# Kernel optimization log

Hardware: AMD Instinct MI355X
Metric: run time of the kernel (lower is better)

Reference implementation:

```python
import jax, jax.numpy as jnp
import numpy as np

CUR, FULL, BS, D = 1024, 2048, 4, 1024
HN, HD = 16, 64
PREV = FULL - CUR
SCALE = 1.0 / HD ** 0.5


def rel_shift(x):
    # x: (bs, hn, cur, full) -> TXL relative shift over last two dims
    b, h, q, k = x.shape
    x = jnp.pad(x, ((0, 0), (0, 0), (0, 0), (1, 0)))  # (b,h,q,k+1)
    x = x.reshape(b, h, k + 1, q)[:, :, 1:, :]
    return x.reshape(b, h, q, k)


def setup_inputs() -> dict:
    key = jax.random.key(0)
    ks = jax.random.split(key, 16)
    s = 0.02
    inputs = jax.random.normal(ks[0], (CUR, BS, D), jnp.float32)
    pos_embedding = jax.random.normal(ks[1], (FULL, 1, D), jnp.float32)
    full_input = jax.random.normal(ks[2], (FULL, BS, D), jnp.float32)
    # causal mask: query i (absolute pos i+PREV) cannot attend to key j > i+PREV
    i = jnp.arange(CUR)[:, None]
    j = jnp.arange(FULL)[None, :]
    mask = (j > i + PREV)[:, :, None]  # (cur, full, 1) bool
    W_kv = jax.random.normal(ks[3], (D, 2 * HN * HD), jnp.float32) * s
    b_kv = jnp.zeros((2 * HN * HD,), jnp.float32)
    W_q = jax.random.normal(ks[4], (D, HN * HD), jnp.float32) * s
    b_q = jnp.zeros((HN * HD,), jnp.float32)
    W_pos = jax.random.normal(ks[5], (D, HN * HD), jnp.float32) * s
    b_pos = jnp.zeros((HN * HD,), jnp.float32)
    W_proj = jax.random.normal(ks[6], (HN * HD, D), jnp.float32) * s
    b_proj = jnp.zeros((D,), jnp.float32)
    u = jax.random.normal(ks[7], (HN, HD), jnp.float32) * s
    v = jax.random.normal(ks[8], (HN, HD), jnp.float32) * s
    return dict(inputs=inputs, pos_embedding=pos_embedding, full_input=full_input,
                u=u, v=v, mask=mask, W_kv=W_kv, b_kv=b_kv, W_q=W_q, b_q=b_q,
                W_pos=W_pos, b_pos=b_pos, W_proj=W_proj, b_proj=b_proj)


def reference(inputs, pos_embedding, full_input, u, v, mask,
              W_kv, b_kv, W_q, b_q, W_pos, b_pos, W_proj, b_proj):
    cur, bs, _ = inputs.shape
    full = full_input.shape[0]
    kv = full_input @ W_kv + b_kv                      # (full, bs, 2*hn*hd)
    k, val = jnp.split(kv, 2, axis=-1)
    k = k.reshape(full, bs, HN, HD)
    val = val.reshape(full, bs, HN, HD)
    q = (inputs @ W_q + b_q).reshape(cur, bs, HN, HD)
    r = (pos_embedding @ W_pos + b_pos).reshape(full, HN, HD)
    content = jnp.einsum('ibhd,jbhd->bhij', q + u, k)   # (bs,hn,cur,full)
    position = jnp.einsum('ibhd,jhd->bhij', q + v, r)
    position = rel_shift(position)
    attn = (content + position) * SCALE
    attn = jnp.where(mask[None, :, :, 0][:, None, :, :], -jnp.inf, attn)
    attn = jax.nn.softmax(attn, axis=-1)
    out = jnp.einsum('bhij,jbhd->ibhd', attn, val).reshape(cur, bs, HN * HD)
    return out @ W_proj + b_proj
```

## Files before the change

kernel.cpp:

```cpp
#include <hip/hip_runtime.h>


typedef _Float16 half8 __attribute__((ext_vector_type(8)));
typedef _Float16 half4v __attribute__((ext_vector_type(4)));
typedef float f32x4 __attribute__((ext_vector_type(4)));

typedef const __attribute__((address_space(1))) void* gas_ptr;
typedef __attribute__((address_space(3))) void* las_ptr;

__device__ __forceinline__ void load_lds16(const void* g, void* l) {
  __builtin_amdgcn_global_load_lds((gas_ptr)g, (las_ptr)l, 16, 0, 0);
}

__global__ __launch_bounds__(256) void prep(
    const float* __restrict__ inputs, const float* __restrict__ full_inp,
    const float* __restrict__ pos_emb, const float* __restrict__ Wq,
    const float* __restrict__ Wkv, const float* __restrict__ Wpos,
    const float* __restrict__ Wproj, _Float16* __restrict__ o_in,
    _Float16* __restrict__ o_full, _Float16* __restrict__ o_pos,
    _Float16* __restrict__ owq, _Float16* __restrict__ owkv,
    _Float16* __restrict__ owpos, _Float16* __restrict__ owproj) {
  __shared__ _Float16 tile[64][65];
  const int bx = blockIdx.x;
  const int t = threadIdx.x;
  if (bx < 14336) {
    size_t g = (size_t)bx * 256 + t;
    const float* src;
    _Float16* dst;
    size_t sg;
    if (g < (1u << 20)) {
      const int rd = (int)(g >> 8), b = rd >> 10, i = rd & 1023;
      src = inputs; dst = o_in;
      sg = ((size_t)(i * 4 + b) << 8) + (g & 255);
    } else if (g < (3u << 20)) {
      const size_t gd = g - (1u << 20);
      const int rd = (int)(gd >> 8), b = rd >> 11, j = rd & 2047;
      src = full_inp; dst = o_full;
      sg = ((size_t)(j * 4 + b) << 8) + (gd & 255);
      float4 vv = *(const float4*)(src + sg * 4);
      half4v hh;
      hh[0] = (_Float16)vv.x; hh[1] = (_Float16)vv.y;
      hh[2] = (_Float16)vv.z; hh[3] = (_Float16)vv.w;
      *(half4v*)(dst + gd * 4) = hh;
      return;
    } else {
      const size_t gd = g - (3u << 20);
      float4 vv = *(const float4*)(pos_emb + gd * 4);
      half4v hh;
      hh[0] = (_Float16)vv.x; hh[1] = (_Float16)vv.y;
      hh[2] = (_Float16)vv.z; hh[3] = (_Float16)vv.w;
      *(half4v*)(o_pos + gd * 4) = hh;
      return;
    }
    float4 vv = *(const float4*)(src + sg * 4);
    half4v hh;
    hh[0] = (_Float16)vv.x; hh[1] = (_Float16)vv.y;
    hh[2] = (_Float16)vv.z; hh[3] = (_Float16)vv.w;
    *(half4v*)(dst + (g & ((1u << 20) - 1)) * 4) = hh;
    return;
  }
  const int wb = bx - 14336;
  const float* W;
  _Float16* Wt;
  int N, tidx;
  if (wb < 256) { W = Wq; Wt = owq; N = 1024; tidx = wb; }
  else if (wb < 768) { W = Wkv; Wt = owkv; N = 2048; tidx = wb - 256; }
  else if (wb < 1024) { W = Wpos; Wt = owpos; N = 1024; tidx = wb - 768; }
  else { W = Wproj; Wt = owproj; N = 1024; tidx = wb - 1024; }
  const int K = 1024;
  const int n0 = (tidx % (N >> 6)) * 64, k0 = (tidx / (N >> 6)) * 64;
  const int rr = t >> 2, cc = (t & 3) * 16;
#pragma unroll
  for (int i = 0; i < 4; ++i) {
    float4 v = *(const float4*)&W[(size_t)(k0 + rr) * N + n0 + cc + i * 4];
    tile[rr][cc + i * 4 + 0] = (_Float16)v.x;
    tile[rr][cc + i * 4 + 1] = (_Float16)v.y;
    tile[rr][cc + i * 4 + 2] = (_Float16)v.z;
    tile[rr][cc + i * 4 + 3] = (_Float16)v.w;
  }
  __syncthreads();
  const int n = t >> 2, kc = (t & 3) * 16;
#pragma unroll
  for (int i = 0; i < 4; ++i) {
    half4v h;
    h[0] = tile[kc + i * 4 + 0][n];
    h[1] = tile[kc + i * 4 + 1][n];
    h[2] = tile[kc + i * 4 + 2][n];
    h[3] = tile[kc + i * 4 + 3][n];
    *(half4v*)&Wt[(size_t)(n0 + n) * K + k0 + kc + i * 4] = h;
  }
}

__global__ __launch_bounds__(256, 2) void gemm3(
    const _Float16* __restrict__ Aq, const _Float16* __restrict__ Akv,
    const _Float16* __restrict__ Ar, const _Float16* __restrict__ Btq,
    const _Float16* __restrict__ Btkv, const _Float16* __restrict__ Btr,
    const float* __restrict__ bq, const float* __restrict__ bkv,
    const float* __restrict__ br, const float* __restrict__ uu,
    _Float16* __restrict__ qfu, _Float16* __restrict__ kf,
    _Float16* __restrict__ vfT, _Float16* __restrict__ rf) {
  __shared__ _Float16 smem[128 * 66];
  _Float16* As = smem;
  _Float16* Bs = smem + 4096;
  const int gb = blockIdx.x;
  const _Float16* A;
  const _Float16* Bt;
  const float* bias;
  int mode, bm, bn;
  if (gb < 256) {
    mode = 1; A = Aq; Bt = Btq; bias = bq;
    bn = (gb & 7) * 128; bm = (gb >> 3) * 128;
  } else if (gb < 1280) {
    mode = 2; A = Akv; Bt = Btkv; bias = bkv;
    const int j = gb - 256;
    bn = (j & 15) * 128; bm = (j >> 4) * 128;
  } else {
    mode = 3; A = Ar; Bt = Btr; bias = br;
    const int j = gb - 1280;
    bn = (j & 7) * 128; bm = (j >> 3) * 128;
  }
  const int K = 1024;
  const int t = threadIdx.x, w = t >> 6, l = t & 63;
  const int l15 = l & 15, l4 = l >> 4;
  const int wm = (w >> 1) * 64, wn = (w & 1) * 64;

  f32x4 acc[4][4];
  const f32x4 z4 = {0.f, 0.f, 0.f, 0.f};
#pragma unroll
  for (int i = 0; i < 4; ++i)
#pragma unroll
    for (int j = 0; j < 4; ++j) acc[i][j] = z4;

  const char* Abase = (const char*)A + (size_t)bm * K * 2;
  const char* Bbase = (const char*)Bt + (size_t)bn * K * 2;

  for (int k0 = 0; k0 < K; k0 += 32) {
    __syncthreads();
#pragma unroll
    for (int iss = 0; iss < 2; ++iss) {
      const int off = w * 1024 + iss * 4096 + l * 16;
      const int row = off >> 6, kb = off & 63;
      load_lds16(Abase + (size_t)row * (K * 2) + k0 * 2 + kb,
                 (char*)As + off);
      load_lds16(Bbase + (size_t)row * (K * 2) + k0 * 2 + kb,
                 (char*)Bs + off);
    }
    __syncthreads();
    half8 af[4], bf[4];
#pragma unroll
    for (int mt = 0; mt < 4; ++mt)
      af[mt] = *(const half8*)&As[(wm + mt * 16 + l15) * 32 + l4 * 8];
#pragma unroll
    for (int nt = 0; nt < 4; ++nt)
      bf[nt] = *(const half8*)&Bs[(wn + nt * 16 + l15) * 32 + l4 * 8];
#pragma unroll
    for (int mt = 0; mt < 4; ++mt)
#pragma unroll
      for (int nt = 0; nt < 4; ++nt)
        acc[mt][nt] = __builtin_amdgcn_mfma_f32_16x16x32_f16(
            af[mt], bf[nt], acc[mt][nt], 0, 0, 0);
  }

  if (mode == 2 && bn >= 1024) {
    const int b = bm >> 11, j0m = bm & 2047;
    const int hbase = (bn - 1024) >> 6;
#pragma unroll
    for (int ch = 0; ch < 2; ++ch) {
      __syncthreads();
      if (((wn >> 6) & 1) == ch) {
#pragma unroll
        for (int mt = 0; mt < 4; ++mt)
#pragma unroll
          for (int r = 0; r < 4; ++r) {
            const int rowl = wm + mt * 16 + l4 * 4 + r;
#pragma unroll
            for (int nt = 0; nt < 4; ++nt) {
              const int coll = nt * 16 + l15;
              smem[rowl * 66 + coll] =
                  (_Float16)(acc[mt][nt][r] + bias[bn + wn + coll]);
            }
          }
      }
      __syncthreads();
#pragma unroll
      for (int it = 0; it < 4; ++it) {
        const int c = t + 256 * it;
        const int d = c >> 4, ck = c & 15;
        half8 v8;
#pragma unroll
        for (int z = 0; z < 8; ++z) v8[z] = smem[(ck * 8 + z) * 66 + d];
        *(half8*)&vfT[(((size_t)(b * 16 + hbase + ch) * 64 + d) << 11) + j0m +
                      ck * 8] = v8;
      }
    }
    return;
  }

#pragma unroll
  for (int mt = 0; mt < 4; ++mt)
#pragma unroll
    for (int r = 0; r < 4; ++r) {
      const int rowl = wm + mt * 16 + l4 * 4 + r;
#pragma unroll
      for (int nt = 0; nt < 4; ++nt) {
        const int col = bn + wn + nt * 16 + l15;
        const float val = acc[mt][nt][r] + bias[col];
        if (mode == 1) {
          const int b = bm >> 10, i0m = bm & 1023;
          const int h = col >> 6, d = col & 63;
          qfu[(((size_t)(b * 16 + h) * 1024 + i0m + rowl) << 6) + d] =
              (_Float16)((val + uu[col]) * 0.125f);
        } else if (mode == 2) {
          const int b = bm >> 11, j0m = bm & 2047;
          const int h = col >> 6, d = col & 63;
          kf[(((size_t)(b * 16 + h) * 2048 + j0m + rowl) << 6) + d] =
              (_Float16)val;
        } else {
          const int h = col >> 6, d = col & 63;
          rf[(((size_t)h * 2048 + bm + rowl) << 6) + d] = (_Float16)val;
        }
      }
    }
}

__global__ __launch_bounds__(256, 2) void gemm_proj(
    const _Float16* __restrict__ A, const _Float16* __restrict__ Bt,
    const float* __restrict__ bias, float* __restrict__ out0, int M, int N,
    int K) {
  __shared__ _Float16 As[128 * 32];
  __shared__ _Float16 Bs[128 * 32];
  const int t = threadIdx.x, w = t >> 6, l = t & 63;
  const int l15 = l & 15, l4 = l >> 4;
  const int bm = blockIdx.y * 128, bn = blockIdx.x * 128;
  const int wm = (w >> 1) * 64, wn = (w & 1) * 64;

  f32x4 acc[4][4];
  const f32x4 z4 = {0.f, 0.f, 0.f, 0.f};
#pragma unroll
  for (int i = 0; i < 4; ++i)
#pragma unroll
    for (int j = 0; j < 4; ++j) acc[i][j] = z4;

  const char* Abase = (const char*)A + (size_t)bm * K * 2;
  const char* Bbase = (const char*)Bt + (size_t)bn * K * 2;

  for (int k0 = 0; k0 < K; k0 += 32) {
    __syncthreads();
#pragma unroll
    for (int iss = 0; iss < 2; ++iss) {
      const int off = w * 1024 + iss * 4096 + l * 16;
      const int row = off >> 6, kb = off & 63;
      load_lds16(Abase + (size_t)row * (K * 2) + k0 * 2 + kb,
                 (char*)As + off);
      load_lds16(Bbase + (size_t)row * (K * 2) + k0 * 2 + kb,
                 (char*)Bs + off);
    }
    __syncthreads();
    half8 af[4], bf[4];
#pragma unroll
    for (int mt = 0; mt < 4; ++mt)
      af[mt] = *(const half8*)&As[(wm + mt * 16 + l15) * 32 + l4 * 8];
#pragma unroll
    for (int nt = 0; nt < 4; ++nt)
      bf[nt] = *(const half8*)&Bs[(wn + nt * 16 + l15) * 32 + l4 * 8];
#pragma unroll
    for (int mt = 0; mt < 4; ++mt)
#pragma unroll
      for (int nt = 0; nt < 4; ++nt)
        acc[mt][nt] = __builtin_amdgcn_mfma_f32_16x16x32_f16(
            af[mt], bf[nt], acc[mt][nt], 0, 0, 0);
  }

#pragma unroll
  for (int mt = 0; mt < 4; ++mt)
#pragma unroll
    for (int r = 0; r < 4; ++r) {
      const int row = bm + wm + mt * 16 + l4 * 4 + r;
#pragma unroll
      for (int nt = 0; nt < 4; ++nt) {
        const int col = bn + wn + nt * 16 + l15;
        out0[(size_t)row * N + col] = acc[mt][nt][r] + bias[col];
      }
    }
}

__global__ __launch_bounds__(256, 2) void attn_mfma(
    const _Float16* __restrict__ qfu,
    const _Float16* __restrict__ kf,
    const _Float16* __restrict__ vfT,
    const _Float16* __restrict__ rf,
    const float* __restrict__ u,
    const float* __restrict__ v,
    _Float16* __restrict__ attn_out)
{
  __shared__ _Float16 ks[64 * 64];
  __shared__ _Float16 vts[64 * 64];
  __shared__ _Float16 rs[256 * 64];
  __shared__ _Float16 pA[2][4][16 * 64];

  const int t = threadIdx.x, w = t >> 6, l = t & 63;
  const int l15 = l & 15, l4 = l >> 4;
  const int id = blockIdx.x;
  const int bh = ((id >> 3) & 7) * 8 + (id & 7);
  const int qt = id >> 6;
  const int bx = (qt < 4) ? (7 - qt) : (qt - 4);
  const int i0 = bx * 128;
  const int h = bh & 15, b = bh >> 4;

  const char* kfb = (const char*)(kf + (((size_t)bh * 2048) << 6));
  const char* vg = (const char*)(vfT + (((size_t)bh) << 17));
  const char* rg = (const char*)(rf + (((size_t)h) << 17));

  half8 qa0[2], qa1[2], qv0[2], qv1[2];
  {
    half8 dl0, dl1;
#pragma unroll
    for (int z = 0; z < 8; ++z) {
      const int di = l4 * 8 + z;
      dl0[z] = (_Float16)(0.125f * (v[h * 64 + di] - u[h * 64 + di]));
      dl1[z] = (_Float16)(0.125f * (v[h * 64 + 32 + di] - u[h * 64 + 32 + di]));
    }
#pragma unroll
    for (int g = 0; g < 2; ++g) {
      const size_t qo =
          (((size_t)bh * 1024 + i0 + 64 * g + w * 16 + l15) << 6) + l4 * 8;
      qa0[g] = *(const half8*)(qfu + qo);
      qa1[g] = *(const half8*)(qfu + qo + 32);
      qv0[g] = qa0[g] + dl0;
      qv1[g] = qa1[g] + dl1;
    }
  }
  const f32x4 z4 = {0.f, 0.f, 0.f, 0.f};
  f32x4 o[2][4];
  float lsum[2][4];
#pragma unroll
  for (int g = 0; g < 2; ++g)
#pragma unroll
    for (int nt = 0; nt < 4; ++nt) { o[g][nt] = z4; lsum[g][nt] = 0.f; }

  const int mb0 = 960 - i0;
  const int njt = 2 * bx + 18;

#pragma unroll
  for (int iss = 0; iss < 6; ++iss) {
    const int off = w * 1024 + iss * 4096 + l * 16;
    const int q = off >> 7;
    const int cph = (off >> 4) & 7;
    const int slot = (mb0 - 64 + q) & 255;
    int m = mb0 - 64 + q;
    m = m < 2047 ? m : 2047;
    load_lds16(rg + (size_t)m * 128 + ((cph ^ (slot & 7)) << 4),
               (char*)rs + slot * 128 + cph * 16);
  }

  for (int jt = 0; jt < njt; ++jt) {
    const int j0 = jt * 64;
    const int m_base = j0 - i0 + 960;
    __syncthreads();
    {
      const char* kg = kfb + (size_t)j0 * 128;
#pragma unroll
      for (int iss = 0; iss < 2; ++iss) {
        const int off = w * 1024 + iss * 4096 + l * 16;
        const int row = off >> 7;
        const int cph = (off >> 4) & 7;
        const int sw = ((cph ^ (row & 7)) << 4);
        load_lds16(kg + (size_t)row * 128 + sw, (char*)ks + off);
        load_lds16(vg + (size_t)row * 4096 + (size_t)j0 * 2 + sw,
                   (char*)vts + off);
      }
    }
    if (jt > 0) {
      const int m0 = m_base + 64;
#pragma unroll
      for (int iss = 0; iss < 2; ++iss) {
        const int off = w * 1024 + iss * 4096 + l * 16;
        const int q = off >> 7;
        const int cph = (off >> 4) & 7;
        const int slot = (m0 + q) & 255;
        int m = m0 + q;
        m = m < 2047 ? m : 2047;
        load_lds16(rg + (size_t)m * 128 + ((cph ^ (slot & 7)) << 4),
                   (char*)rs + slot * 128 + cph * 16);
      }
    }
    __syncthreads();

    f32x4 sc[2][4];
#pragma unroll
    for (int nt = 0; nt < 4; ++nt) {
      const int row = nt * 16 + l15;
      const int rsw = row & 7;
      const half8 b0 = *(const half8*)&ks[row * 64 + ((l4 ^ rsw) * 8)];
      const half8 b1 = *(const half8*)&ks[row * 64 + (((4 + l4) ^ rsw) * 8)];
#pragma unroll
      for (int g = 0; g < 2; ++g) {
        f32x4 cc = z4;
        cc = __builtin_amdgcn_mfma_f32_16x16x32_f16(qa0[g], b0, cc, 0, 0, 0);
        cc = __builtin_amdgcn_mfma_f32_16x16x32_f16(qa1[g], b1, cc, 0, 0, 0);
        sc[g][nt] = cc;
      }
    }

#pragma unroll
    for (int g = 0; g < 2; ++g) {
      const int cw = i0 + 64 * g - j0 + 1024 + 16 * w;
      if (g == 0 && cw < -15) continue;
      const int mbg = m_base - 64 * g;
      f32x4 accP[5];
#pragma unroll
      for (int p = 0; p < 5; ++p) {
        const int m = mbg + (3 - w + p) * 16 + l15;
        const int slot = m & 255;
        const int ssw = slot & 7;
        const half8 b0 = *(const half8*)&rs[slot * 64 + ((l4 ^ ssw) * 8)];
        const half8 b1 = *(const half8*)&rs[slot * 64 + (((4 + l4) ^ ssw) * 8)];
        f32x4 cc = z4;
        cc = __builtin_amdgcn_mfma_f32_16x16x32_f16(qv0[g], b0, cc, 0, 0, 0);
        cc = __builtin_amdgcn_mfma_f32_16x16x32_f16(qv1[g], b1, cc, 0, 0, 0);
        accP[p] = cc;
      }
      if (cw >= 63) {
#pragma unroll
        for (int r = 0; r < 4; ++r) {
          const int thr = 4 * l4 + r;
          const int srcl = (l4 << 4) | ((15 + l15 - thr) & 15);
          float rot[5];
#pragma unroll
          for (int p = 0; p < 5; ++p) rot[p] = __shfl(accP[p][r], srcl, 64);
          float esum = 0.f;
          const int sw2 = (thr & 7) * 8;
#pragma unroll
          for (int nt = 0; nt < 4; ++nt) {
            const float pv = (l15 <= thr) ? rot[nt] : rot[nt + 1];
            const float e = __expf(sc[g][nt][r] + pv);
            esum += e;
            pA[g][w][thr * 64 + ((16 * nt + l15) ^ sw2)] = (_Float16)e;
          }
          lsum[g][r] += esum;
        }
      } else {
#pragma unroll
        for (int r = 0; r < 4; ++r) {
          const int thr = 4 * l4 + r;
          const int srcl = (l4 << 4) | ((15 + l15 - thr) & 15);
          float rot[5];
#pragma unroll
          for (int p = 0; p < 5; ++p) rot[p] = __shfl(accP[p][r], srcl, 64);
          float esum = 0.f;
          const int sw2 = (thr & 7) * 8;
#pragma unroll
          for (int nt = 0; nt < 4; ++nt) {
            const float pv = (l15 <= thr) ? rot[nt] : rot[nt + 1];
            const bool masked = (16 * nt + l15) > (cw + thr);
            const float e = masked ? 0.f : __expf(sc[g][nt][r] + pv);
            esum += e;
            pA[g][w][thr * 64 + ((16 * nt + l15) ^ sw2)] = (_Float16)e;
          }
          lsum[g][r] += esum;
        }
      }
    }

    const bool act0 = (i0 - j0 + 1024 + 16 * w) >= -15;
#pragma unroll
    for (int kk = 0; kk < 2; ++kk) {
      const int aoff = l15 * 64 + ((kk * 32 + l4 * 8) ^ ((l15 & 7) * 8));
      half8 a81 = *(const half8*)&pA[1][w][aoff];
      half8 a80;
      if (act0) a80 = *(const half8*)&pA[0][w][aoff];
#pragma unroll
      for (int nt = 0; nt < 4; ++nt) {
        const int row = nt * 16 + l15;
        const half8 b8 =
            *(const half8*)&vts[row * 64 + ((((kk << 2) + l4) ^ (row & 7)) * 8)];
        if (act0)
          o[0][nt] =
              __builtin_amdgcn_mfma_f32_16x16x32_f16(a80, b8, o[0][nt], 0, 0, 0);
        o[1][nt] =
            __builtin_amdgcn_mfma_f32_16x16x32_f16(a81, b8, o[1][nt], 0, 0, 0);
      }
    }
  }

#pragma unroll
  for (int g = 0; g < 2; ++g)
#pragma unroll
    for (int r = 0; r < 4; ++r) {
      float s = lsum[g][r];
      s += __shfl_xor(s, 1, 64);
      s += __shfl_xor(s, 2, 64);
      s += __shfl_xor(s, 4, 64);
      s += __shfl_xor(s, 8, 64);
      const float inv = 1.0f / s;
      const int i = i0 + 64 * g + w * 16 + l4 * 4 + r;
      const size_t base = ((size_t)i * 4 + b) * 1024 + h * 64;
#pragma unroll
      for (int nt = 0; nt < 4; ++nt)
        attn_out[base + nt * 16 + l15] = (_Float16)(o[g][nt][r] * inv);
    }
}

extern "C" void kernel_launch(void* const* d_in, const int* in_sizes, int n_in,
                              void* d_out, int out_size, void* d_ws,
                              size_t ws_size, hipStream_t stream) {
  const float* inputs   = (const float*)d_in[0];
  const float* pos_emb  = (const float*)d_in[1];
  const float* full_inp = (const float*)d_in[2];
  const float* u        = (const float*)d_in[3];
  const float* v        = (const float*)d_in[4];
  const float* W_kv   = (const float*)d_in[6];
  const float* b_kv   = (const float*)d_in[7];
  const float* W_q    = (const float*)d_in[8];
  const float* b_q    = (const float*)d_in[9];
  const float* W_pos  = (const float*)d_in[10];
  const float* b_pos  = (const float*)d_in[11];
  const float* W_proj = (const float*)d_in[12];
  const float* b_proj = (const float*)d_in[13];
  float* out = (float*)d_out;

  char* ws = (char*)d_ws;
  const size_t MB = 1024 * 1024;
  _Float16* in_q_h    = (_Float16*)(ws);
  _Float16* in_full_h = (_Float16*)(ws + 8 * MB);
  _Float16* in_pos_h  = (_Float16*)(ws + 24 * MB);
  _Float16* attn_h    = (_Float16*)(ws + 28 * MB);
  _Float16* wq_t      = (_Float16*)(ws + 36 * MB);
  _Float16* wkv_t     = (_Float16*)(ws + 38 * MB);
  _Float16* wpos_t    = (_Float16*)(ws + 42 * MB);
  _Float16* wproj_t   = (_Float16*)(ws + 44 * MB);
  _Float16* qfu       = (_Float16*)(ws + 46 * MB);
  _Float16* kf        = (_Float16*)(ws + 54 * MB);
  _Float16* vfT       = (_Float16*)(ws + 70 * MB);
  _Float16* rf        = (_Float16*)(ws + 86 * MB);

  const dim3 blk(256);
  prep<<<dim3(15616), blk, 0, stream>>>(inputs, full_inp, pos_emb, W_q, W_kv,
                                        W_pos, W_proj, in_q_h, in_full_h,
                                        in_pos_h, wq_t, wkv_t, wpos_t, wproj_t);
  gemm3<<<dim3(1408), blk, 0, stream>>>(in_q_h, in_full_h, in_pos_h, wq_t,
                                        wkv_t, wpos_t, b_q, b_kv, b_pos, u,
                                        qfu, kf, vfT, rf);
  attn_mfma<<<dim3(512), blk, 0, stream>>>(qfu, kf, vfT, rf, u, v, attn_h);
  gemm_proj<<<dim3(8, 32), blk, 0, stream>>>(attn_h, wproj_t, b_proj, out,
                                             4096, 1024, 1024);
}
```

Before: 333.1 us.

## Double GEMM K-tile to 64 with XOR-swizzled LDS and batch prep conversion

The two MFMA GEMM kernels now stage a 64-wide K slice per iteration instead of 32. This halves the number of barrier-synchronised load rounds. An XOR swizzle on 16-byte chunks in the global-to-LDS copy and the fragment reads is meant to avoid LDS bank conflicts with the wider rows. The prep kernel's elementwise fp32-to-fp16 conversion is also restructured so each of 2048 blocks handles 7 chunks in an unrolled loop, which cuts the block count. In exchange, LDS use per block doubles, which could limit occupancy.

```diff
diff --git a/kernel.cpp b/kernel.cpp
--- a/kernel.cpp
+++ b/kernel.cpp
@@ -23,43 +23,36 @@
   __shared__ _Float16 tile[64][65];
   const int bx = blockIdx.x;
   const int t = threadIdx.x;
-  if (bx < 14336) {
-    size_t g = (size_t)bx * 256 + t;
-    const float* src;
-    _Float16* dst;
-    size_t sg;
-    if (g < (1u << 20)) {
-      const int rd = (int)(g >> 8), b = rd >> 10, i = rd & 1023;
-      src = inputs; dst = o_in;
-      sg = ((size_t)(i * 4 + b) << 8) + (g & 255);
-    } else if (g < (3u << 20)) {
-      const size_t gd = g - (1u << 20);
-      const int rd = (int)(gd >> 8), b = rd >> 11, j = rd & 2047;
-      src = full_inp; dst = o_full;
-      sg = ((size_t)(j * 4 + b) << 8) + (gd & 255);
-      float4 vv = *(const float4*)(src + sg * 4);
+  if (bx < 2048) {
+#pragma unroll
+    for (int it = 0; it < 7; ++it) {
+      const size_t g = (size_t)bx * 256 + t + (size_t)it * (2048 * 256);
+      float4 vv;
+      _Float16* dptr;
+      if (g < (1u << 20)) {
+        const int rd = (int)(g >> 8), b = rd >> 10, i = rd & 1023;
+        const size_t sg = ((size_t)(i * 4 + b) << 8) + (g & 255);
+        vv = *(const float4*)(inputs + sg * 4);
+        dptr = o_in + g * 4;
+      } else if (g < (3u << 20)) {
+        const size_t gd = g - (1u << 20);
+        const int rd = (int)(gd >> 8), b = rd >> 11, j = rd & 2047;
+        const size_t sg = ((size_t)(j * 4 + b) << 8) + (gd & 255);
+        vv = *(const float4*)(full_inp + sg * 4);
+        dptr = o_full + gd * 4;
+      } else {
+        const size_t gd = g - (3u << 20);
+        vv = *(const float4*)(pos_emb + gd * 4);
+        dptr = o_pos + gd * 4;
+      }
       half4v hh;
       hh[0] = (_Float16)vv.x; hh[1] = (_Float16)vv.y;
       hh[2] = (_Float16)vv.z; hh[3] = (_Float16)vv.w;
-      *(half4v*)(dst + gd * 4) = hh;
-      return;
-    } else {
-      const size_t gd = g - (3u << 20);
-      float4 vv = *(const float4*)(pos_emb + gd * 4);
-      half4v hh;
-      hh[0] = (_Float16)vv.x; hh[1] = (_Float16)vv.y;
-      hh[2] = (_Float16)vv.z; hh[3] = (_Float16)vv.w;
-      *(half4v*)(o_pos + gd * 4) = hh;
-      return;
-    }
-    float4 vv = *(const float4*)(src + sg * 4);
-    half4v hh;
-    hh[0] = (_Float16)vv.x; hh[1] = (_Float16)vv.y;
-    hh[2] = (_Float16)vv.z; hh[3] = (_Float16)vv.w;
-    *(half4v*)(dst + (g & ((1u << 20) - 1)) * 4) = hh;
+      *(half4v*)dptr = hh;
+    }
     return;
   }
-  const int wb = bx - 14336;
+  const int wb = bx - 2048;
   const float* W;
   _Float16* Wt;
   int N, tidx;
@@ -99,9 +92,9 @@
     const float* __restrict__ br, const float* __restrict__ uu,
     _Float16* __restrict__ qfu, _Float16* __restrict__ kf,
     _Float16* __restrict__ vfT, _Float16* __restrict__ rf) {
-  __shared__ _Float16 smem[128 * 66];
+  __shared__ _Float16 smem[128 * 128];
   _Float16* As = smem;
-  _Float16* Bs = smem + 4096;
+  _Float16* Bs = smem + 8192;
   const int gb = blockIdx.x;
   const _Float16* A;
   const _Float16* Bt;
@@ -134,31 +127,34 @@
   const char* Abase = (const char*)A + (size_t)bm * K * 2;
   const char* Bbase = (const char*)Bt + (size_t)bn * K * 2;
 
-  for (int k0 = 0; k0 < K; k0 += 32) {
+  for (int k0 = 0; k0 < K; k0 += 64) {
     __syncthreads();
 #pragma unroll
-    for (int iss = 0; iss < 2; ++iss) {
-      const int off = w * 1024 + iss * 4096 + l * 16;
-      const int row = off >> 6, kb = off & 63;
-      load_lds16(Abase + (size_t)row * (K * 2) + k0 * 2 + kb,
-                 (char*)As + off);
-      load_lds16(Bbase + (size_t)row * (K * 2) + k0 * 2 + kb,
-                 (char*)Bs + off);
+    for (int iss = 0; iss < 4; ++iss) {
+      const int off = w * 4096 + iss * 1024 + l * 16;
+      const int row = off >> 7;
+      const int sw = ((((off >> 4) & 7) ^ (row & 7)) << 4);
+      load_lds16(Abase + (size_t)row * (K * 2) + k0 * 2 + sw, (char*)As + off);
+      load_lds16(Bbase + (size_t)row * (K * 2) + k0 * 2 + sw, (char*)Bs + off);
     }
     __syncthreads();
-    half8 af[4], bf[4];
-#pragma unroll
-    for (int mt = 0; mt < 4; ++mt)
-      af[mt] = *(const half8*)&As[(wm + mt * 16 + l15) * 32 + l4 * 8];
-#pragma unroll
-    for (int nt = 0; nt < 4; ++nt)
-      bf[nt] = *(const half8*)&Bs[(wn + nt * 16 + l15) * 32 + l4 * 8];
-#pragma unroll
-    for (int mt = 0; mt < 4; ++mt)
+#pragma unroll
+    for (int ks = 0; ks < 2; ++ks) {
+      const int ch = ((ks * 4 + l4) ^ (l15 & 7)) * 8;
+      half8 af[4], bf[4];
+#pragma unroll
+      for (int mt = 0; mt < 4; ++mt)
+        af[mt] = *(const half8*)&As[(wm + mt * 16 + l15) * 64 + ch];
 #pragma unroll
       for (int nt = 0; nt < 4; ++nt)
-        acc[mt][nt] = __builtin_amdgcn_mfma_f32_16x16x32_f16(
-            af[mt], bf[nt], acc[mt][nt], 0, 0, 0);
+        bf[nt] = *(const half8*)&Bs[(wn + nt * 16 + l15) * 64 + ch];
+#pragma unroll
+      for (int mt = 0; mt < 4; ++mt)
+#pragma unroll
+        for (int nt = 0; nt < 4; ++nt)
+          acc[mt][nt] = __builtin_amdgcn_mfma_f32_16x16x32_f16(
+              af[mt], bf[nt], acc[mt][nt], 0, 0, 0);
+    }
   }
 
   if (mode == 2 && bn >= 1024) {
@@ -227,8 +223,8 @@
     const _Float16* __restrict__ A, const _Float16* __restrict__ Bt,
     const float* __restrict__ bias, float* __restrict__ out0, int M, int N,
     int K) {
-  __shared__ _Float16 As[128 * 32];
-  __shared__ _Float16 Bs[128 * 32];
+  __shared__ _Float16 As[128 * 64];
+  __shared__ _Float16 Bs[128 * 64];
   const int t = threadIdx.x, w = t >> 6, l = t & 63;
   const int l15 = l & 15, l4 = l >> 4;
   const int bm = blockIdx.y * 128, bn = blockIdx.x * 128;
@@ -244,31 +240,34 @@
   const char* Abase = (const char*)A + (size_t)bm * K * 2;
   const char* Bbase = (const char*)Bt + (size_t)bn * K * 2;
 
-  for (int k0 = 0; k0 < K; k0 += 32) {
+  for (int k0 = 0; k0 < K; k0 += 64) {
     __syncthreads();
 #pragma unroll
-    for (int iss = 0; iss < 2; ++iss) {
-      const int off = w * 1024 + iss * 4096 + l * 16;
-      const int row = off >> 6, kb = off & 63;
-      load_lds16(Abase + (size_t)row * (K * 2) + k0 * 2 + kb,
-                 (char*)As + off);
-      load_lds16(Bbase + (size_t)row * (K * 2) + k0 * 2 + kb,
-                 (char*)Bs + off);
+    for (int iss = 0; iss < 4; ++iss) {
+      const int off = w * 4096 + iss * 1024 + l * 16;
+      const int row = off >> 7;
+      const int sw = ((((off >> 4) & 7) ^ (row & 7)) << 4);
+      load_lds16(Abase + (size_t)row * (K * 2) + k0 * 2 + sw, (char*)As + off);
+      load_lds16(Bbase + (size_t)row * (K * 2) + k0 * 2 + sw, (char*)Bs + off);
     }
     __syncthreads();
-    half8 af[4], bf[4];
-#pragma unroll
-    for (int mt = 0; mt < 4; ++mt)
-      af[mt] = *(const half8*)&As[(wm + mt * 16 + l15) * 32 + l4 * 8];
-#pragma unroll
-    for (int nt = 0; nt < 4; ++nt)
-      bf[nt] = *(const half8*)&Bs[(wn + nt * 16 + l15) * 32 + l4 * 8];
-#pragma unroll
-    for (int mt = 0; mt < 4; ++mt)
+#pragma unroll
+    for (int ks = 0; ks < 2; ++ks) {
+      const int ch = ((ks * 4 + l4) ^ (l15 & 7)) * 8;
+      half8 af[4], bf[4];
+#pragma unroll
+      for (int mt = 0; mt < 4; ++mt)
+        af[mt] = *(const half8*)&As[(wm + mt * 16 + l15) * 64 + ch];
 #pragma unroll
       for (int nt = 0; nt < 4; ++nt)
-        acc[mt][nt] = __builtin_amdgcn_mfma_f32_16x16x32_f16(
-            af[mt], bf[nt], acc[mt][nt], 0, 0, 0);
+        bf[nt] = *(const half8*)&Bs[(wn + nt * 16 + l15) * 64 + ch];
+#pragma unroll
+      for (int mt = 0; mt < 4; ++mt)
+#pragma unroll
+        for (int nt = 0; nt < 4; ++nt)
+          acc[mt][nt] = __builtin_amdgcn_mfma_f32_16x16x32_f16(
+              af[mt], bf[nt], acc[mt][nt], 0, 0, 0);
+    }
   }
 
 #pragma unroll
@@ -535,9 +534,9 @@
   _Float16* rf        = (_Float16*)(ws + 86 * MB);
 
   const dim3 blk(256);
-  prep<<<dim3(15616), blk, 0, stream>>>(inputs, full_inp, pos_emb, W_q, W_kv,
-                                        W_pos, W_proj, in_q_h, in_full_h,
-                                        in_pos_h, wq_t, wkv_t, wpos_t, wproj_t);
+  prep<<<dim3(3328), blk, 0, stream>>>(inputs, full_inp, pos_emb, W_q, W_kv,
+                                       W_pos, W_proj, in_q_h, in_full_h,
+                                       in_pos_h, wq_t, wkv_t, wpos_t, wproj_t);
   gemm3<<<dim3(1408), blk, 0, stream>>>(in_q_h, in_full_h, in_pos_h, wq_t,
                                         wkv_t, wpos_t, b_q, b_kv, b_pos, u,
                                         qfu, kf, vfT, rf);
```

Measured after the change: 335.0 us. No clear change (+0.6%).
